# Performance work log

Hardware: AMD Instinct MI355X
Metric: run time of the kernel (lower is better)

## Reference

```python
import jax, jax.numpy as jnp
import numpy as np

LAGS = 1
LAYER_DIM = (8, 8)
HIDDEN = 64
B, T = 256, 513
D = sum(LAYER_DIM)  # 16


def _leaky(v):
    # torch nn.LeakyReLU default negative_slope = 0.01
    return jnp.where(v >= 0, v, 0.01 * v)


def _mlp(v, W1, b1, W2, b2, W3, b3):
    # MLP2: Linear -> LeakyReLU -> Linear -> LeakyReLU -> Linear(out=1); scalar output
    h = _leaky(W1 @ v + b1)
    h = _leaky(W2 @ h + b2)
    return (W3 @ h + b3)[0]


def _block(inputs, W1, b1, W2, b2, W3, b3):
    # inputs: [dim, N, in_dim]; params stacked over the per-variable axis [dim, ...]
    # value_and_grad fuses the residual forward with the Jacobian row (output dim == 1,
    # so the full jacfwd row equals the gradient wrt the input vector).
    f = jax.value_and_grad(_mlp, argnums=0)
    f = jax.vmap(f, in_axes=(0, None, None, None, None, None, None))  # over N samples
    f = jax.vmap(f)                                                    # over dim variables
    return f(inputs, W1, b1, W2, b2, W3, b3)  # out: [dim, N], grad: [dim, N, in_dim]


def _init_mlp(key, n, in_dim, hidden):
    ks = jax.random.split(key, 6)
    s1 = 1.0 / np.sqrt(in_dim)
    s2 = 1.0 / np.sqrt(hidden)
    u = jax.random.uniform
    return (u(ks[0], (n, hidden, in_dim), minval=-s1, maxval=s1),
            u(ks[1], (n, hidden), minval=-s1, maxval=s1),
            u(ks[2], (n, hidden, hidden), minval=-s2, maxval=s2),
            u(ks[3], (n, hidden), minval=-s2, maxval=s2),
            u(ks[4], (n, 1, hidden), minval=-s2, maxval=s2),
            u(ks[5], (n, 1), minval=-s2, maxval=s2))


def setup_inputs() -> dict:
    key = jax.random.key(0)
    k1, k2, k3, k4 = jax.random.split(key, 4)
    x = jax.random.normal(k1, (B, T, D), dtype=jnp.float32)
    alphas = jax.random.normal(k2, (D,), dtype=jnp.float32)  # unused by forward (kept for signature fidelity)
    p0 = _init_mlp(k3, LAYER_DIM[0], LAGS * LAYER_DIM[0] + 1, HIDDEN)               # in_dim = 9
    p1 = _init_mlp(k4, LAYER_DIM[1], LAGS * LAYER_DIM[1] + LAYER_DIM[0] + 1, HIDDEN)  # in_dim = 17
    d = {"x": x, "alphas": alphas}
    names = ["W1", "b1", "W2", "b2", "W3", "b3"]
    for nm, v in zip(names, p0):
        d["l0_" + nm] = v
    for nm, v in zip(names, p1):
        d["l1_" + nm] = v
    return d


def _forward(x, alphas, params):
    Bsz, Tlen, Din = x.shape
    L = LAGS
    # torch unfold(dim=1, size=L+1, step=1) + swapaxes(2,3): [B, T-L, L+1, D]
    win = jnp.stack([x[:, i:Tlen - L + i] for i in range(L + 1)], axis=2)
    win = win.reshape(-1, L + 1, Din)
    xx = win[:, -1, :]                       # [N, D]  (torch keeps [N,1,D])
    yy = win[:, :-1, :].reshape(-1, L * Din)  # [N, L*D]
    N = xx.shape[0]

    delay_right = Din
    hiera = (0, 0)
    res_blocks, hist = [], []
    logdet = jnp.zeros((N,), x.dtype)
    for l, dim in enumerate(LAYER_DIM):
        delay_left = delay_right - dim
        Pa_d = yy[:, delay_left:delay_right]                      # [N, dim] (L=1)
        Pa_d_b = jnp.broadcast_to(Pa_d[None], (dim,) + Pa_d.shape)
        if l == 0:
            # per-variable scalar xx[:, delay_left + i]
            xcol = xx[:, delay_left:delay_right].T[:, :, None]    # [dim, N, 1]
            inputs = jnp.concatenate([Pa_d_b, xcol], axis=-1)     # [dim, N, L*dim+1]
        else:
            hl, hr = hiera
            Pa_h = xx[:, hl:hr]                                   # [N, prev_dim]
            Pa_h_b = jnp.broadcast_to(Pa_h[None], (dim,) + Pa_h.shape)
            xcol = xx[:, :dim].T[:, :, None]                      # torch uses xx[:, :, i]
            inputs = jnp.concatenate([Pa_d_b, Pa_h_b, xcol], axis=-1)
        out, grad = _block(inputs, *params[l])                    # [dim,N], [dim,N,in]
        res_blocks.append(out.T)                                  # [N, dim]
        logdet = logdet + jnp.sum(jnp.log(jnp.abs(grad[..., -1])), axis=0)
        hist.append(grad[:, :, None, :-1])                        # stacked hist_jac: [dim, N, 1, in-1]
        hiera = (delay_left, delay_right)
        delay_right -= dim
    residuals = jnp.concatenate(res_blocks, axis=-1).reshape(Bsz, -1, Din)
    sumlog = jnp.sum(logdet.reshape(Bsz, -1), axis=1)
    return residuals, sumlog, hist


def reference(x, alphas, l0_W1, l0_b1, l0_W2, l0_b2, l0_W3, l0_b3,
              l1_W1, l1_b1, l1_W2, l1_b2, l1_W3, l1_b3):
    params = [(l0_W1, l0_b1, l0_W2, l0_b2, l0_W3, l0_b3),
              (l1_W1, l1_b1, l1_W2, l1_b2, l1_W3, l1_b3)]
    residuals, sumlog, hist = _forward(x, alphas, params)
    return (residuals, sumlog, hist[0], hist[1])
```

## Files before the change

kernel.cpp:

```cpp
#include <hip/hip_runtime.h>
#include <hip/hip_bf16.h>
#include <cmath>


namespace {

using bf16x8 = __attribute__((ext_vector_type(8))) short;
using f32x4  = __attribute__((ext_vector_type(4))) float;
using f32x2  = __attribute__((ext_vector_type(2))) float;
using bf2    = __attribute__((ext_vector_type(2))) __bf16;
using u32x2  = __attribute__((ext_vector_type(2))) unsigned;
using u32x4  = __attribute__((ext_vector_type(4))) unsigned;

constexpr int NB = 256, NT = 512, TROW = 513, DIN = 16, HID = 64;
constexpr int NSAMP = NB * NT;
constexpr size_t OFF_SUMLOG = (size_t)NSAMP * DIN;
constexpr size_t OFF_H0     = OFF_SUMLOG + NB;
constexpr size_t OFF_H1     = OFF_H0 + (size_t)8 * NSAMP * 8;

struct SMem {
    alignas(16) char frag[3 * 8192];
    float sresW[256];
    float slogW[4];
};

__device__ __forceinline__ short b16(float f) {
    return __builtin_bit_cast(short, (__bf16)f);
}
__device__ __forceinline__ unsigned pk2(float a, float b) {
    f32x2 t{a, b};
    return __builtin_bit_cast(unsigned, __builtin_convertvector(t, bf2));
}
__device__ __forceinline__ bf16x8 mkfrag(unsigned a, unsigned b, unsigned c, unsigned d) {
    u32x4 t{a, b, c, d};
    return __builtin_bit_cast(bf16x8, t);
}
__device__ __forceinline__ f32x4 mfma16(bf16x8 a, bf16x8 b, f32x4 c) {
    return __builtin_amdgcn_mfma_f32_16x16x32_bf16(a, b, c, 0, 0, 0);
}

template<int L, int IN>
__device__ __forceinline__ void mlp_impl(
    SMem& sm, int d, int b,
    const float* __restrict__ x,
    const float* __restrict__ gW1, const float* __restrict__ gb1,
    const float* __restrict__ gW2, const float* __restrict__ gb2,
    const float* __restrict__ gW3, const float* __restrict__ gb3,
    float* __restrict__ out)
{
    const int tid = threadIdx.x;
    const int w = tid >> 6, lane = tid & 63;
    const int q = lane >> 4, r = lane & 15;

    const int rbase = (q * 1024 + r * 16)
                    ^ ((((q & 3) << 1) ^ ((r >> 3) & 1)) << 4);
    const int q4w = 2 * w + (q >> 1);
    const int wbase = (q4w * 1024 + r * 16 + (q & 1) * 8)
                    ^ ((((q4w & 3) << 1) ^ ((r >> 3) & 1)) << 4);
    char* fr = sm.frag;

    bf16x8 aW1;
    {
        const float* p = gW1 + (size_t)(d * HID + 16 * w + r) * IN;
        #pragma unroll
        for (int e = 0; e < 8; ++e) {
            int k = 8 * q + e;
            aW1[e] = (k < IN) ? b16(p[k]) : (short)0;
        }
    }
    bf16x8 aW2[2], aW2T[2];
    #pragma unroll
    for (int ks = 0; ks < 2; ++ks) {
        const float* p = gW2 + (size_t)(d * HID + 16 * w + r) * HID + 32 * ks + 8 * q;
        #pragma unroll
        for (int e = 0; e < 8; ++e) aW2[ks][e] = b16(p[e]);
        const float* pt = gW2 + (size_t)d * HID * HID
                        + (size_t)(32 * ks + 8 * q) * HID + 16 * w + r;
        #pragma unroll
        for (int e = 0; e < 8; ++e) aW2T[ks][e] = b16(pt[(size_t)e * HID]);
    }
    constexpr int NMT = (IN > 16) ? 2 : 1;
    bf16x8 aW1T[NMT][2];
    #pragma unroll
    for (int mt = 0; mt < NMT; ++mt) {
        const int i = 16 * mt + r;
        #pragma unroll
        for (int ks = 0; ks < 2; ++ks) {
            const float* pt = gW1 + (size_t)d * HID * IN
                            + (size_t)(32 * ks + 8 * q) * IN + i;
            #pragma unroll
            for (int e = 0; e < 8; ++e)
                aW1T[mt][ks][e] = (i < IN) ? b16(pt[(size_t)e * IN]) : (short)0;
        }
    }
    const f32x4 c1init = *reinterpret_cast<const f32x4*>(gb1 + d * HID + 16 * w + 4 * q);
    const f32x4 c2init = *reinterpret_cast<const f32x4*>(gb2 + d * HID + 16 * w + 4 * q);
    const f32x4 w3r    = *reinterpret_cast<const f32x4*>(gW3 + d * HID + 16 * w + 4 * q);
    f32x4 w3s;
    #pragma unroll
    for (int e = 0; e < 4; ++e) w3s[e] = 0.01f * w3r[e];
    const float b3v = gb3[d];

    const float* xb = x + (size_t)b * TROW * DIN;
    float lgacc = 0.0f;

    for (int ps = 0; ps < 8; ++ps) {
        const int tbase = ps * 64;
        float d1v[16];

        #pragma unroll
        for (int g = 0; g < 4; ++g) {
            const float* xr = xb + (size_t)(tbase + 16 * g + r) * DIN;
            float f0=0,f1=0,f2=0,f3=0,f4=0,f5=0,f6=0,f7=0;
            if constexpr (L == 0) {
                if (q == 0) {
                    f32x4 u0 = *reinterpret_cast<const f32x4*>(xr + 8);
                    f32x4 u1 = *reinterpret_cast<const f32x4*>(xr + 12);
                    f0=u0[0]; f1=u0[1]; f2=u0[2]; f3=u0[3];
                    f4=u1[0]; f5=u1[1]; f6=u1[2]; f7=u1[3];
                } else if (q == 1) {
                    f0 = xr[DIN + 8 + d];
                }
            } else {
                if (q == 0) {
                    f32x4 u0 = *reinterpret_cast<const f32x4*>(xr);
                    f32x4 u1 = *reinterpret_cast<const f32x4*>(xr + 4);
                    f0=u0[0]; f1=u0[1]; f2=u0[2]; f3=u0[3];
                    f4=u1[0]; f5=u1[1]; f6=u1[2]; f7=u1[3];
                } else if (q == 1) {
                    f32x4 u0 = *reinterpret_cast<const f32x4*>(xr + 24);
                    f32x4 u1 = *reinterpret_cast<const f32x4*>(xr + 28);
                    f0=u0[0]; f1=u0[1]; f2=u0[2]; f3=u0[3];
                    f4=u1[0]; f5=u1[1]; f6=u1[2]; f7=u1[3];
                } else if (q == 2) {
                    f0 = xr[DIN + d];
                }
            }
            bf16x8 bv = mkfrag(pk2(f0,f1), pk2(f2,f3), pk2(f4,f5), pk2(f6,f7));
            f32x4 acc = mfma16(aW1, bv, c1init);
            float hh[4];
            #pragma unroll
            for (int e = 0; e < 4; ++e) {
                float dd = (acc[e] >= 0.0f) ? 1.0f : 0.01f;
                d1v[g * 4 + e] = dd;
                hh[e] = acc[e] * dd;
            }
            *reinterpret_cast<u32x2*>(fr + wbase + g * 256) =
                u32x2{pk2(hh[0], hh[1]), pk2(hh[2], hh[3])};
        }
        __syncthreads();

        #pragma unroll
        for (int g = 0; g < 4; ++g) {
            f32x4 acc = c2init;
            acc = mfma16(aW2[0], *reinterpret_cast<const bf16x8*>(fr + rbase + g*256), acc);
            acc = mfma16(aW2[1], *reinterpret_cast<const bf16x8*>(fr + rbase + 4096 + g*256), acc);
            float pr = 0.0f, u2v[4];
            #pragma unroll
            for (int e = 0; e < 4; ++e) {
                u2v[e] = (acc[e] >= 0.0f) ? w3r[e] : w3s[e];
                pr = fmaf(u2v[e], acc[e], pr);
            }
            pr += __shfl_xor(pr, 16, 64);
            pr += __shfl_xor(pr, 32, 64);
            if (q == 0) sm.sresW[w * 64 + 16 * g + r] = pr;
            *reinterpret_cast<u32x2*>(fr + 8192 + wbase + g * 256) =
                u32x2{pk2(u2v[0], u2v[1]), pk2(u2v[2], u2v[3])};
        }
        __syncthreads();

        #pragma unroll
        for (int g = 0; g < 4; ++g) {
            f32x4 acc = {0.0f, 0.0f, 0.0f, 0.0f};
            acc = mfma16(aW2T[0], *reinterpret_cast<const bf16x8*>(fr + 8192 + rbase + g*256), acc);
            acc = mfma16(aW2T[1], *reinterpret_cast<const bf16x8*>(fr + 8192 + rbase + 4096 + g*256), acc);
            float u0 = acc[0] * d1v[g*4+0], u1 = acc[1] * d1v[g*4+1];
            float u2 = acc[2] * d1v[g*4+2], u3 = acc[3] * d1v[g*4+3];
            *reinterpret_cast<u32x2*>(fr + 16384 + wbase + g * 256) =
                u32x2{pk2(u0, u1), pk2(u2, u3)};
        }
        __syncthreads();

        {
            const size_t nglob = (size_t)b * NT + tbase + 16 * w + r;
            bf16x8 bu0 = *reinterpret_cast<const bf16x8*>(fr + 16384 + rbase + w * 256);
            bf16x8 bu1 = *reinterpret_cast<const bf16x8*>(fr + 16384 + rbase + 4096 + w * 256);
            f32x4 g0 = {0.0f, 0.0f, 0.0f, 0.0f};
            g0 = mfma16(aW1T[0][0], bu0, g0);
            g0 = mfma16(aW1T[0][1], bu1, g0);
            if constexpr (L == 1) {
                f32x4 g1 = {0.0f, 0.0f, 0.0f, 0.0f};
                g1 = mfma16(aW1T[1][0], bu0, g1);
                g1 = mfma16(aW1T[1][1], bu1, g1);
                *reinterpret_cast<f32x4*>(out + OFF_H1 + ((size_t)d * NSAMP + nglob) * 16 + 4 * q) = g0;
                if (q == 0) lgacc += logf(fabsf(g1[0]));
            } else {
                if (q < 2)
                    *reinterpret_cast<f32x4*>(out + OFF_H0 + ((size_t)d * NSAMP + nglob) * 8 + 4 * q) = g0;
                if (q == 2) lgacc += logf(fabsf(g0[0]));
            }
        }
        if (tid < 64) {
            float rs = sm.sresW[tid] + sm.sresW[64 + tid]
                     + sm.sresW[128 + tid] + sm.sresW[192 + tid] + b3v;
            out[((size_t)b * NT + tbase + tid) * DIN + (L * 8 + d)] = rs;
        }
    }

    float v = lgacc;
    #pragma unroll
    for (int off = 1; off < 64; off <<= 1) v += __shfl_xor(v, off, 64);
    if (lane == 0) sm.slogW[w] = v;
    __syncthreads();
    if (tid == 0)
        atomicAdd(out + OFF_SUMLOG + b,
                  sm.slogW[0] + sm.slogW[1] + sm.slogW[2] + sm.slogW[3]);
}

__global__ void zero_sumlog_kernel(float* __restrict__ out) {
    out[OFF_SUMLOG + threadIdx.x] = 0.0f;
}

__global__ __launch_bounds__(256, 3) void mlp_mfma_kernel(
    const float* __restrict__ x,
    const float* __restrict__ l0W1, const float* __restrict__ l0b1,
    const float* __restrict__ l0W2, const float* __restrict__ l0b2,
    const float* __restrict__ l0W3, const float* __restrict__ l0b3,
    const float* __restrict__ l1W1, const float* __restrict__ l1b1,
    const float* __restrict__ l1W2, const float* __restrict__ l1b2,
    const float* __restrict__ l1W3, const float* __restrict__ l1b3,
    float* __restrict__ out)
{
    __shared__ SMem sm;
    const int xcd = blockIdx.x & 7;
    const int idx = blockIdx.x >> 3;
    const int b   = xcd * 32 + (idx & 31);
    const int uld = idx >> 5;
    if (uld < 8)
        mlp_impl<0, 9>(sm, uld, b, x, l0W1, l0b1, l0W2, l0b2, l0W3, l0b3, out);
    else
        mlp_impl<1, 17>(sm, uld - 8, b, x, l1W1, l1b1, l1W2, l1b2, l1W3, l1b3, out);
}

}

extern "C" void kernel_launch(void* const* d_in, const int* in_sizes, int n_in,
                              void* d_out, int out_size, void* d_ws, size_t ws_size,
                              hipStream_t stream) {
    const float* x = (const float*)d_in[0];
    float* out = (float*)d_out;

    zero_sumlog_kernel<<<1, 256, 0, stream>>>(out);
    mlp_mfma_kernel<<<4096, 256, 0, stream>>>(
        x,
        (const float*)d_in[2],  (const float*)d_in[3],  (const float*)d_in[4],
        (const float*)d_in[5],  (const float*)d_in[6],  (const float*)d_in[7],
        (const float*)d_in[8],  (const float*)d_in[9],  (const float*)d_in[10],
        (const float*)d_in[11], (const float*)d_in[12], (const float*)d_in[13],
        out);
}
```

Baseline: 148.7 us.

## Give each wave its own 16 samples and full weights, removing block barriers

The work split changes so that each wave processes its own 16 time-steps through all 64 hidden units, holding every weight tile in registers. Intermediate activations pass through a per-wave LDS scratch area, so the three __syncthreads per pass and the cross-wave residual reduction are no longer needed. The layer-1 bias is folded into the W1 fragment through a constant-1 input column, and launch bounds drop from 3 to 2 blocks per CU to make room for the larger register footprint. The cost is much higher VGPR pressure and lower occupancy. The LDS layout also loses its XOR swizzle, which may bring back bank conflicts.

Measured after the change: 165.5 us. +11.2%, slower.

```diff
diff --git a/kernel.cpp b/kernel.cpp
--- a/kernel.cpp
+++ b/kernel.cpp
@@ -19,8 +19,7 @@
 constexpr size_t OFF_H1     = OFF_H0 + (size_t)8 * NSAMP * 8;
 
 struct SMem {
-    alignas(16) char frag[3 * 8192];
-    float sresW[256];
+    alignas(16) char scr[4][6144];
     float slogW[4];
 };
 
@@ -37,6 +36,13 @@
 }
 __device__ __forceinline__ f32x4 mfma16(bf16x8 a, bf16x8 b, f32x4 c) {
     return __builtin_amdgcn_mfma_f32_16x16x32_bf16(a, b, c, 0, 0, 0);
+}
+__device__ __forceinline__ void wrD(char* buf, int m, int q, int r, f32x4 v) {
+    u32x2 t{pk2(v[0], v[1]), pk2(v[2], v[3])};
+    *reinterpret_cast<u32x2*>(buf + ((2 * m + (q >> 1)) << 8) + (r << 4) + ((q & 1) << 3)) = t;
+}
+__device__ __forceinline__ bf16x8 rdB(const char* buf, int ks, int q, int r) {
+    return *reinterpret_cast<const bf16x8*>(buf + (((ks << 2) + q) << 8) + (r << 4));
 }
 
 template<int L, int IN>
@@ -51,33 +57,36 @@
     const int tid = threadIdx.x;
     const int w = tid >> 6, lane = tid & 63;
     const int q = lane >> 4, r = lane & 15;
-
-    const int rbase = (q * 1024 + r * 16)
-                    ^ ((((q & 3) << 1) ^ ((r >> 3) & 1)) << 4);
-    const int q4w = 2 * w + (q >> 1);
-    const int wbase = (q4w * 1024 + r * 16 + (q & 1) * 8)
-                    ^ ((((q4w & 3) << 1) ^ ((r >> 3) & 1)) << 4);
-    char* fr = sm.frag;
-
-    bf16x8 aW1;
-    {
-        const float* p = gW1 + (size_t)(d * HID + 16 * w + r) * IN;
+    char* scr = sm.scr[w];
+
+    bf16x8 aW1[4];
+    #pragma unroll
+    for (int m = 0; m < 4; ++m) {
+        const float* p  = gW1 + (size_t)(d * HID + 16 * m + r) * IN;
+        const float  bb = gb1[d * HID + 16 * m + r];
         #pragma unroll
         for (int e = 0; e < 8; ++e) {
             int k = 8 * q + e;
-            aW1[e] = (k < IN) ? b16(p[k]) : (short)0;
-        }
-    }
-    bf16x8 aW2[2], aW2T[2];
-    #pragma unroll
-    for (int ks = 0; ks < 2; ++ks) {
-        const float* p = gW2 + (size_t)(d * HID + 16 * w + r) * HID + 32 * ks + 8 * q;
-        #pragma unroll
-        for (int e = 0; e < 8; ++e) aW2[ks][e] = b16(p[e]);
-        const float* pt = gW2 + (size_t)d * HID * HID
-                        + (size_t)(32 * ks + 8 * q) * HID + 16 * w + r;
-        #pragma unroll
-        for (int e = 0; e < 8; ++e) aW2T[ks][e] = b16(pt[(size_t)e * HID]);
+            float v = (k < IN) ? p[k] : ((k == IN) ? bb : 0.0f);
+            aW1[m][e] = b16(v);
+        }
+    }
+    bf16x8 aW2[4][2], aW2T[4][2];
+    #pragma unroll
+    for (int m = 0; m < 4; ++m) {
+        #pragma unroll
+        for (int ks = 0; ks < 2; ++ks) {
+            const float* p = gW2 + (size_t)d * HID * HID
+                           + (size_t)(16 * m + r) * HID + 32 * ks + 8 * q;
+            f32x4 u0 = *reinterpret_cast<const f32x4*>(p);
+            f32x4 u1 = *reinterpret_cast<const f32x4*>(p + 4);
+            aW2[m][ks] = mkfrag(pk2(u0[0], u0[1]), pk2(u0[2], u0[3]),
+                                pk2(u1[0], u1[1]), pk2(u1[2], u1[3]));
+            const float* pt = gW2 + (size_t)d * HID * HID
+                            + (size_t)(32 * ks + 8 * q) * HID + 16 * m + r;
+            #pragma unroll
+            for (int e = 0; e < 8; ++e) aW2T[m][ks][e] = b16(pt[(size_t)e * HID]);
+        }
     }
     constexpr int NMT = (IN > 16) ? 2 : 1;
     bf16x8 aW1T[NMT][2];
@@ -93,124 +102,115 @@
                 aW1T[mt][ks][e] = (i < IN) ? b16(pt[(size_t)e * IN]) : (short)0;
         }
     }
-    const f32x4 c1init = *reinterpret_cast<const f32x4*>(gb1 + d * HID + 16 * w + 4 * q);
-    const f32x4 c2init = *reinterpret_cast<const f32x4*>(gb2 + d * HID + 16 * w + 4 * q);
-    const f32x4 w3r    = *reinterpret_cast<const f32x4*>(gW3 + d * HID + 16 * w + 4 * q);
-    f32x4 w3s;
-    #pragma unroll
-    for (int e = 0; e < 4; ++e) w3s[e] = 0.01f * w3r[e];
+    f32x4 c2i[4], w3r[4], w3s[4];
+    #pragma unroll
+    for (int m = 0; m < 4; ++m) {
+        c2i[m] = *reinterpret_cast<const f32x4*>(gb2 + d * HID + 16 * m + 4 * q);
+        w3r[m] = *reinterpret_cast<const f32x4*>(gW3 + d * HID + 16 * m + 4 * q);
+        #pragma unroll
+        for (int e = 0; e < 4; ++e) w3s[m][e] = 0.01f * w3r[m][e];
+    }
     const float b3v = gb3[d];
 
     const float* xb = x + (size_t)b * TROW * DIN;
-    float lgacc = 0.0f;
+    float lg = 0.0f;
+    const f32x4 zero = {0.0f, 0.0f, 0.0f, 0.0f};
 
     for (int ps = 0; ps < 8; ++ps) {
-        const int tbase = ps * 64;
-        float d1v[16];
-
-        #pragma unroll
-        for (int g = 0; g < 4; ++g) {
-            const float* xr = xb + (size_t)(tbase + 16 * g + r) * DIN;
-            float f0=0,f1=0,f2=0,f3=0,f4=0,f5=0,f6=0,f7=0;
-            if constexpr (L == 0) {
-                if (q == 0) {
-                    f32x4 u0 = *reinterpret_cast<const f32x4*>(xr + 8);
-                    f32x4 u1 = *reinterpret_cast<const f32x4*>(xr + 12);
-                    f0=u0[0]; f1=u0[1]; f2=u0[2]; f3=u0[3];
-                    f4=u1[0]; f5=u1[1]; f6=u1[2]; f7=u1[3];
-                } else if (q == 1) {
-                    f0 = xr[DIN + 8 + d];
-                }
-            } else {
-                if (q == 0) {
-                    f32x4 u0 = *reinterpret_cast<const f32x4*>(xr);
-                    f32x4 u1 = *reinterpret_cast<const f32x4*>(xr + 4);
-                    f0=u0[0]; f1=u0[1]; f2=u0[2]; f3=u0[3];
-                    f4=u1[0]; f5=u1[1]; f6=u1[2]; f7=u1[3];
-                } else if (q == 1) {
-                    f32x4 u0 = *reinterpret_cast<const f32x4*>(xr + 24);
-                    f32x4 u1 = *reinterpret_cast<const f32x4*>(xr + 28);
-                    f0=u0[0]; f1=u0[1]; f2=u0[2]; f3=u0[3];
-                    f4=u1[0]; f5=u1[1]; f6=u1[2]; f7=u1[3];
-                } else if (q == 2) {
-                    f0 = xr[DIN + d];
-                }
-            }
-            bf16x8 bv = mkfrag(pk2(f0,f1), pk2(f2,f3), pk2(f4,f5), pk2(f6,f7));
-            f32x4 acc = mfma16(aW1, bv, c1init);
-            float hh[4];
+        const int t = ps * 64 + 16 * w + r;
+        const float* yyp = xb + (size_t)t * DIN;
+
+        float f0=0, f1=0, f2=0, f3=0, f4=0, f5=0, f6=0, f7=0;
+        if constexpr (L == 0) {
+            if (q == 0) {
+                f32x4 u0 = *reinterpret_cast<const f32x4*>(yyp + 8);
+                f32x4 u1 = *reinterpret_cast<const f32x4*>(yyp + 12);
+                f0=u0[0]; f1=u0[1]; f2=u0[2]; f3=u0[3];
+                f4=u1[0]; f5=u1[1]; f6=u1[2]; f7=u1[3];
+            } else if (q == 1) {
+                f0 = yyp[DIN + 8 + d];
+                f1 = 1.0f;
+            }
+        } else {
+            if (q == 0) {
+                f32x4 u0 = *reinterpret_cast<const f32x4*>(yyp);
+                f32x4 u1 = *reinterpret_cast<const f32x4*>(yyp + 4);
+                f0=u0[0]; f1=u0[1]; f2=u0[2]; f3=u0[3];
+                f4=u1[0]; f5=u1[1]; f6=u1[2]; f7=u1[3];
+            } else if (q == 1) {
+                f32x4 u0 = *reinterpret_cast<const f32x4*>(yyp + 24);
+                f32x4 u1 = *reinterpret_cast<const f32x4*>(yyp + 28);
+                f0=u0[0]; f1=u0[1]; f2=u0[2]; f3=u0[3];
+                f4=u1[0]; f5=u1[1]; f6=u1[2]; f7=u1[3];
+            } else if (q == 2) {
+                f0 = yyp[DIN + d];
+                f1 = 1.0f;
+            }
+        }
+        bf16x8 bv = mkfrag(pk2(f0,f1), pk2(f2,f3), pk2(f4,f5), pk2(f6,f7));
+
+        f32x4 d1v[4];
+        #pragma unroll
+        for (int m = 0; m < 4; ++m) {
+            f32x4 acc = mfma16(aW1[m], bv, zero);
+            f32x4 h;
             #pragma unroll
             for (int e = 0; e < 4; ++e) {
                 float dd = (acc[e] >= 0.0f) ? 1.0f : 0.01f;
-                d1v[g * 4 + e] = dd;
-                hh[e] = acc[e] * dd;
-            }
-            *reinterpret_cast<u32x2*>(fr + wbase + g * 256) =
-                u32x2{pk2(hh[0], hh[1]), pk2(hh[2], hh[3])};
-        }
-        __syncthreads();
-
-        #pragma unroll
-        for (int g = 0; g < 4; ++g) {
-            f32x4 acc = c2init;
-            acc = mfma16(aW2[0], *reinterpret_cast<const bf16x8*>(fr + rbase + g*256), acc);
-            acc = mfma16(aW2[1], *reinterpret_cast<const bf16x8*>(fr + rbase + 4096 + g*256), acc);
-            float pr = 0.0f, u2v[4];
+                d1v[m][e] = dd;
+                h[e] = acc[e] * dd;
+            }
+            wrD(scr, m, q, r, h);
+        }
+        bf16x8 bh0 = rdB(scr, 0, q, r), bh1 = rdB(scr, 1, q, r);
+
+        float pr = 0.0f;
+        #pragma unroll
+        for (int m = 0; m < 4; ++m) {
+            f32x4 acc = mfma16(aW2[m][0], bh0, c2i[m]);
+            acc = mfma16(aW2[m][1], bh1, acc);
+            f32x4 u2;
             #pragma unroll
             for (int e = 0; e < 4; ++e) {
-                u2v[e] = (acc[e] >= 0.0f) ? w3r[e] : w3s[e];
-                pr = fmaf(u2v[e], acc[e], pr);
-            }
-            pr += __shfl_xor(pr, 16, 64);
-            pr += __shfl_xor(pr, 32, 64);
-            if (q == 0) sm.sresW[w * 64 + 16 * g + r] = pr;
-            *reinterpret_cast<u32x2*>(fr + 8192 + wbase + g * 256) =
-                u32x2{pk2(u2v[0], u2v[1]), pk2(u2v[2], u2v[3])};
-        }
-        __syncthreads();
-
-        #pragma unroll
-        for (int g = 0; g < 4; ++g) {
-            f32x4 acc = {0.0f, 0.0f, 0.0f, 0.0f};
-            acc = mfma16(aW2T[0], *reinterpret_cast<const bf16x8*>(fr + 8192 + rbase + g*256), acc);
-            acc = mfma16(aW2T[1], *reinterpret_cast<const bf16x8*>(fr + 8192 + rbase + 4096 + g*256), acc);
-            float u0 = acc[0] * d1v[g*4+0], u1 = acc[1] * d1v[g*4+1];
-            float u2 = acc[2] * d1v[g*4+2], u3 = acc[3] * d1v[g*4+3];
-            *reinterpret_cast<u32x2*>(fr + 16384 + wbase + g * 256) =
-                u32x2{pk2(u0, u1), pk2(u2, u3)};
-        }
-        __syncthreads();
-
-        {
-            const size_t nglob = (size_t)b * NT + tbase + 16 * w + r;
-            bf16x8 bu0 = *reinterpret_cast<const bf16x8*>(fr + 16384 + rbase + w * 256);
-            bf16x8 bu1 = *reinterpret_cast<const bf16x8*>(fr + 16384 + rbase + 4096 + w * 256);
-            f32x4 g0 = {0.0f, 0.0f, 0.0f, 0.0f};
-            g0 = mfma16(aW1T[0][0], bu0, g0);
-            g0 = mfma16(aW1T[0][1], bu1, g0);
-            if constexpr (L == 1) {
-                f32x4 g1 = {0.0f, 0.0f, 0.0f, 0.0f};
-                g1 = mfma16(aW1T[1][0], bu0, g1);
-                g1 = mfma16(aW1T[1][1], bu1, g1);
-                *reinterpret_cast<f32x4*>(out + OFF_H1 + ((size_t)d * NSAMP + nglob) * 16 + 4 * q) = g0;
-                if (q == 0) lgacc += logf(fabsf(g1[0]));
-            } else {
-                if (q < 2)
-                    *reinterpret_cast<f32x4*>(out + OFF_H0 + ((size_t)d * NSAMP + nglob) * 8 + 4 * q) = g0;
-                if (q == 2) lgacc += logf(fabsf(g0[0]));
-            }
-        }
-        if (tid < 64) {
-            float rs = sm.sresW[tid] + sm.sresW[64 + tid]
-                     + sm.sresW[128 + tid] + sm.sresW[192 + tid] + b3v;
-            out[((size_t)b * NT + tbase + tid) * DIN + (L * 8 + d)] = rs;
-        }
-    }
-
-    float v = lgacc;
-    #pragma unroll
-    for (int off = 1; off < 64; off <<= 1) v += __shfl_xor(v, off, 64);
-    if (lane == 0) sm.slogW[w] = v;
+                u2[e] = (acc[e] >= 0.0f) ? w3r[m][e] : w3s[m][e];
+                pr = fmaf(u2[e], acc[e], pr);
+            }
+            wrD(scr + 2048, m, q, r, u2);
+        }
+        pr += __shfl_xor(pr, 16, 64);
+        pr += __shfl_xor(pr, 32, 64);
+        if (q == 0) out[((size_t)b * NT + t) * DIN + (L * 8 + d)] = pr + b3v;
+        bf16x8 bu0 = rdB(scr + 2048, 0, q, r), bu1 = rdB(scr + 2048, 1, q, r);
+
+        #pragma unroll
+        for (int m = 0; m < 4; ++m) {
+            f32x4 acc = mfma16(aW2T[m][0], bu0, zero);
+            acc = mfma16(aW2T[m][1], bu1, acc);
+            f32x4 u;
+            #pragma unroll
+            for (int e = 0; e < 4; ++e) u[e] = acc[e] * d1v[m][e];
+            wrD(scr + 4096, m, q, r, u);
+        }
+        bf16x8 bg0 = rdB(scr + 4096, 0, q, r), bg1 = rdB(scr + 4096, 1, q, r);
+
+        f32x4 g0 = mfma16(aW1T[0][0], bg0, zero);
+        g0 = mfma16(aW1T[0][1], bg1, g0);
+        const size_t nglob = (size_t)b * NT + t;
+        if constexpr (L == 1) {
+            f32x4 g1 = mfma16(aW1T[1][0], bg0, zero);
+            g1 = mfma16(aW1T[1][1], bg1, g1);
+            *reinterpret_cast<f32x4*>(out + OFF_H1 + ((size_t)d * NSAMP + nglob) * 16 + 4 * q) = g0;
+            if (q == 0) lg += logf(fabsf(g1[0]));
+        } else {
+            if (q < 2)
+                *reinterpret_cast<f32x4*>(out + OFF_H0 + ((size_t)d * NSAMP + nglob) * 8 + 4 * q) = g0;
+            if (q == 2) lg += logf(fabsf(g0[0]));
+        }
+    }
+
+    #pragma unroll
+    for (int off = 1; off < 64; off <<= 1) lg += __shfl_xor(lg, off, 64);
+    if (lane == 0) sm.slogW[w] = lg;
     __syncthreads();
     if (tid == 0)
         atomicAdd(out + OFF_SUMLOG + b,
@@ -221,7 +221,7 @@
     out[OFF_SUMLOG + threadIdx.x] = 0.0f;
 }
 
-__global__ __launch_bounds__(256, 3) void mlp_mfma_kernel(
+__global__ __launch_bounds__(256, 2) void mlp_mfma_kernel(
     const float* __restrict__ x,
     const float* __restrict__ l0W1, const float* __restrict__ l0b1,
     const float* __restrict__ l0W2, const float* __restrict__ l0b2,
```
